# Kernel tuning notes

Hardware: AMD Instinct MI355X
Metric: run time of the kernel (lower is better)

Reference implementation:

```python
import jax, jax.numpy as jnp
import numpy as np

EPS = 1e-6  # floor

def setup_inputs() -> dict:
    key = jax.random.key(0)
    k1, = jax.random.split(key, 1)
    # mel-spectrogram magnitudes: non-negative
    x = jax.random.uniform(k1, (64, 2048, 160, 1), dtype=jnp.float32)  # [B,T,F,C]
    alpha = jnp.array([0.98], dtype=jnp.float32)
    smooth = jnp.array([0.03], dtype=jnp.float32)
    delta = jnp.array([2.0], dtype=jnp.float32)
    root = jnp.array([0.5], dtype=jnp.float32)
    return {"x": x, "alpha": alpha, "smooth": smooth, "delta": delta, "root": root}

def reference(x, alpha, smooth, delta, root):
    # EMA recurrence over time: m[t] = (1 - s) * x[t] + s * m[t-1], m[-1] = 0
    xt = jnp.swapaxes(x, 0, 1)  # [T,B,F,C]

    def step(prev, cur):
        new = (1.0 - smooth) * cur + smooth * prev
        return new, new

    _, smoothed_t = jax.lax.scan(step, jnp.zeros_like(xt[0]), xt)
    smoothed = jnp.swapaxes(smoothed_t, 0, 1)  # [B,T,F,C]

    # PCEN: (x / (eps + M)^alpha + delta)^root - delta^root
    pcen = (x / (EPS + smoothed) ** alpha + delta) ** root - delta ** root
    return pcen
```

## Files before the change

### kernel.cpp

```cpp
#include <hip/hip_runtime.h>
#include <stdint.h>

#define EPS 1e-6f

constexpr int Bq   = 64;
constexpr int Tq   = 2048;
constexpr int Fq   = 160;
constexpr int FQ4  = 40;
constexpr int ROWS = 64;
constexpr int WARM = 8;
constexpr int CH   = 8;
constexpr int TPB  = 320;
constexpr int NTILE = Tq / ROWS;
constexpr int NWG   = Bq * NTILE;
constexpr int TILE_ROWS  = ROWS + WARM;
constexpr int TILE_BYTES = TILE_ROWS * Fq * 4;
constexpr int MAIN_BYTES = ROWS * Fq * 4;

typedef float f4 __attribute__((ext_vector_type(4)));

__device__ __forceinline__ float fast_pow_pos(float b, float e) {
    return __builtin_amdgcn_exp2f(e * __builtin_amdgcn_logf(b));
}

template<bool RSQ>
__device__ __forceinline__ float pcen_one(float xv, float h, float na, float oms,
                                          float r, float d, float droot) {
    float me    = fmaf(oms, h, EPS);
    float ratio = xv * __builtin_amdgcn_exp2f(na * __builtin_amdgcn_logf(me));
    if (RSQ) return __builtin_amdgcn_sqrtf(ratio + d) - droot;
    else     return fast_pow_pos(ratio + d, r) - droot;
}

__device__ __forceinline__ void load_lds_16(const void* g, void* l) {
    __builtin_amdgcn_global_load_lds(
        (const unsigned int __attribute__((address_space(1)))*)(uintptr_t)g,
        (unsigned int __attribute__((address_space(3)))*)(uint32_t)(uintptr_t)l,
        16, 0, 0);
}

template<bool RSQ>
__device__ __forceinline__ void main_loop(const float* __restrict__ lds,
                                          int c, int f, f4 h,
                                          float s, float oms, float na,
                                          float r, float d, float droot,
                                          f4* __restrict__ outr, int gbase) {
#pragma unroll
    for (int j = 0; j < CH; ++j) {
        f4 xv = *(const f4*)&lds[(WARM + c * CH + j) * Fq + f * 4];
        h.x = fmaf(s, h.x, xv.x);
        h.y = fmaf(s, h.y, xv.y);
        h.z = fmaf(s, h.z, xv.z);
        h.w = fmaf(s, h.w, xv.w);
        f4 o;
        o.x = pcen_one<RSQ>(xv.x, h.x, na, oms, r, d, droot);
        o.y = pcen_one<RSQ>(xv.y, h.y, na, oms, r, d, droot);
        o.z = pcen_one<RSQ>(xv.z, h.z, na, oms, r, d, droot);
        o.w = pcen_one<RSQ>(xv.w, h.w, na, oms, r, d, droot);
        __builtin_nontemporal_store(o, &outr[gbase + j * FQ4]);
    }
}

__global__ __launch_bounds__(TPB) void pcen_kernel(
    const float* __restrict__ x,
    const float* __restrict__ alpha_p,
    const float* __restrict__ smooth_p,
    const float* __restrict__ delta_p,
    const float* __restrict__ root_p,
    float* __restrict__ out)
{
    __shared__ __align__(16) float lds[TILE_ROWS * Fq];

    const int wg    = ((blockIdx.x & 7) << 8) | (blockIdx.x >> 3);
    const int tile  = wg % NTILE;
    const int b     = wg / NTILE;
    const int r0    = b * Tq + tile * ROWS;
    const bool first = (tile == 0);

    const int wave = threadIdx.x >> 6;
    const int lane = threadIdx.x & 63;

    {
        const char* src = (const char*)(x + (size_t)(first ? r0 : r0 - WARM) * Fq);
        char*       dst = (char*)lds + (first ? WARM * Fq * 4 : 0);
        const int   per = (first ? MAIN_BYTES : TILE_BYTES) / 1024 / 5;
        for (int i = 0; i < per; ++i) {
            const int off = (wave + 5 * i) * 1024;
            load_lds_16(src + off + lane * 16, dst + off);
        }
    }

    const float s     = smooth_p[0];
    const float a     = alpha_p[0];
    const float d     = delta_p[0];
    const float r     = root_p[0];
    const float oms   = 1.0f - s;
    const float na    = -a;
    const bool  rsq   = (r == 0.5f);
    const float droot = rsq ? __builtin_amdgcn_sqrtf(d) : fast_pow_pos(d, r);

    __syncthreads();

    const int f = threadIdx.x % FQ4;
    const int c = threadIdx.x / FQ4;

    f4 h = (f4){0.f, 0.f, 0.f, 0.f};

    if (!(first && c == 0)) {
#pragma unroll
        for (int j = 0; j < WARM; ++j) {
            f4 xv = *(const f4*)&lds[(c * CH + j) * Fq + f * 4];
            h.x = fmaf(s, h.x, xv.x);
            h.y = fmaf(s, h.y, xv.y);
            h.z = fmaf(s, h.z, xv.z);
            h.w = fmaf(s, h.w, xv.w);
        }
    }

    f4* __restrict__ outr = (f4*)out;
    const int gbase = (r0 + c * CH) * FQ4 + f;

    if (rsq) main_loop<true >(lds, c, f, h, s, oms, na, r, d, droot, outr, gbase);
    else     main_loop<false>(lds, c, f, h, s, oms, na, r, d, droot, outr, gbase);
}

extern "C" void kernel_launch(void* const* d_in, const int* in_sizes, int n_in,
                              void* d_out, int out_size, void* d_ws, size_t ws_size,
                              hipStream_t stream) {
    const float* x      = (const float*)d_in[0];
    const float* alpha  = (const float*)d_in[1];
    const float* smooth = (const float*)d_in[2];
    const float* delta  = (const float*)d_in[3];
    const float* root   = (const float*)d_in[4];
    float* out          = (float*)d_out;

    pcen_kernel<<<NWG, TPB, 0, stream>>>(x, alpha, smooth, delta, root, out);
}
```

Measured before the change: 156.8 us.

## Process four time tiles per block with double-buffered LDS prefetch

```diff
diff --git a/kernel.cpp b/kernel.cpp
--- a/kernel.cpp
+++ b/kernel.cpp
@@ -12,12 +12,16 @@
 constexpr int CH   = 8;
 constexpr int TPB  = 320;
 constexpr int NTILE = Tq / ROWS;
-constexpr int NWG   = Bq * NTILE;
-constexpr int TILE_ROWS  = ROWS + WARM;
-constexpr int TILE_BYTES = TILE_ROWS * Fq * 4;
-constexpr int MAIN_BYTES = ROWS * Fq * 4;
+constexpr int TPG   = 4;
+constexpr int QUADS = NTILE / TPG;
+constexpr int BLKS  = Bq * QUADS;
+constexpr int TILE_F = ROWS * Fq;
 
 typedef float f4 __attribute__((ext_vector_type(4)));
+
+#define SCHED0() __builtin_amdgcn_sched_barrier(0)
+#define BAR() do { SCHED0(); __builtin_amdgcn_s_barrier(); SCHED0(); } while (0)
+#define WAIT_VM8() do { asm volatile("s_waitcnt vmcnt(8)" ::: "memory"); SCHED0(); } while (0)
 
 __device__ __forceinline__ float fast_pow_pos(float b, float e) {
     return __builtin_amdgcn_exp2f(e * __builtin_amdgcn_logf(b));
@@ -32,6 +36,13 @@
     else     return fast_pow_pos(ratio + d, r) - droot;
 }
 
+__device__ __forceinline__ void ema4(f4& h, const f4 xv, float s) {
+    h.x = fmaf(s, h.x, xv.x);
+    h.y = fmaf(s, h.y, xv.y);
+    h.z = fmaf(s, h.z, xv.z);
+    h.w = fmaf(s, h.w, xv.w);
+}
+
 __device__ __forceinline__ void load_lds_16(const void* g, void* l) {
     __builtin_amdgcn_global_load_lds(
         (const unsigned int __attribute__((address_space(1)))*)(uintptr_t)g,
@@ -40,24 +51,75 @@
 }
 
 template<bool RSQ>
-__device__ __forceinline__ void main_loop(const float* __restrict__ lds,
-                                          int c, int f, f4 h,
-                                          float s, float oms, float na,
-                                          float r, float d, float droot,
-                                          f4* __restrict__ outr, int gbase) {
+__device__ __forceinline__ void run(
+    const float* __restrict__ x, float* __restrict__ out,
+    float (* __restrict__ lds)[TILE_F],
+    int r00, bool gwarm, int f, int c, int wave, int lane,
+    float s, float oms, float na, float r, float d, float droot)
+{
+    f4* __restrict__ outr = (f4*)out;
+
+    auto stage = [&](int p, int row0) {
+        const char* src = (const char*)(x + (size_t)row0 * Fq);
+        char*       dst = (char*)&lds[p][0];
 #pragma unroll
-    for (int j = 0; j < CH; ++j) {
-        f4 xv = *(const f4*)&lds[(WARM + c * CH + j) * Fq + f * 4];
-        h.x = fmaf(s, h.x, xv.x);
-        h.y = fmaf(s, h.y, xv.y);
-        h.z = fmaf(s, h.z, xv.z);
-        h.w = fmaf(s, h.w, xv.w);
-        f4 o;
-        o.x = pcen_one<RSQ>(xv.x, h.x, na, oms, r, d, droot);
-        o.y = pcen_one<RSQ>(xv.y, h.y, na, oms, r, d, droot);
-        o.z = pcen_one<RSQ>(xv.z, h.z, na, oms, r, d, droot);
-        o.w = pcen_one<RSQ>(xv.w, h.w, na, oms, r, d, droot);
-        __builtin_nontemporal_store(o, &outr[gbase + j * FQ4]);
+        for (int i = 0; i < 8; ++i) {
+            const int off = (wave + 5 * i) * 1024;
+            load_lds_16(src + off + lane * 16, dst + off);
+        }
+    };
+
+    stage(0, r00);
+
+    f4 wreg[WARM];
+    if (c == 0 && gwarm) {
+        const float* wb = x + (size_t)(r00 - WARM) * Fq + f * 4;
+#pragma unroll
+        for (int j = 0; j < WARM; ++j) wreg[j] = *(const f4*)(wb + j * Fq);
+    }
+
+#pragma unroll
+    for (int t = 0; t < TPG; ++t) {
+        const int p  = t & 1;
+        const int r0 = r00 + t * ROWS;
+
+        f4 h = (f4){0.f, 0.f, 0.f, 0.f};
+        if (c == 0) {
+            if (t == 0) {
+                if (gwarm) {
+#pragma unroll
+                    for (int j = 0; j < WARM; ++j) ema4(h, wreg[j], s);
+                }
+            } else {
+#pragma unroll
+                for (int j = 0; j < WARM; ++j)
+                    ema4(h, *(const f4*)&lds[1 - p][(ROWS - WARM + j) * Fq + f * 4], s);
+            }
+        }
+
+        BAR();
+        if (t + 1 < TPG) stage(1 - p, r0 + ROWS);
+        WAIT_VM8();
+        BAR();
+
+        if (c > 0) {
+#pragma unroll
+            for (int j = 0; j < WARM; ++j)
+                ema4(h, *(const f4*)&lds[p][((c - 1) * CH + j) * Fq + f * 4], s);
+        }
+
+        const int gb = (r0 + c * CH) * FQ4 + f;
+#pragma unroll
+        for (int j = 0; j < CH; ++j) {
+            f4 xv = *(const f4*)&lds[p][(c * CH + j) * Fq + f * 4];
+            ema4(h, xv, s);
+            f4 o;
+            o.x = pcen_one<RSQ>(xv.x, h.x, na, oms, r, d, droot);
+            o.y = pcen_one<RSQ>(xv.y, h.y, na, oms, r, d, droot);
+            o.z = pcen_one<RSQ>(xv.z, h.z, na, oms, r, d, droot);
+            o.w = pcen_one<RSQ>(xv.w, h.w, na, oms, r, d, droot);
+            __builtin_nontemporal_store(o, &outr[gb + j * FQ4]);
+        }
     }
 }
 
@@ -69,26 +131,17 @@
     const float* __restrict__ root_p,
     float* __restrict__ out)
 {
-    __shared__ __align__(16) float lds[TILE_ROWS * Fq];
+    __shared__ __align__(16) float lds[2][TILE_F];
 
-    const int wg    = ((blockIdx.x & 7) << 8) | (blockIdx.x >> 3);
-    const int tile  = wg % NTILE;
-    const int b     = wg / NTILE;
-    const int r0    = b * Tq + tile * ROWS;
-    const bool first = (tile == 0);
+    const int bid = ((blockIdx.x & 7) << 6) | (blockIdx.x >> 3);
+    const int b   = bid / QUADS;
+    const int qd  = bid % QUADS;
+    const int r00 = b * Tq + qd * (TPG * ROWS);
 
+    const int f    = threadIdx.x % FQ4;
+    const int c    = threadIdx.x / FQ4;
     const int wave = threadIdx.x >> 6;
     const int lane = threadIdx.x & 63;
-
-    {
-        const char* src = (const char*)(x + (size_t)(first ? r0 : r0 - WARM) * Fq);
-        char*       dst = (char*)lds + (first ? WARM * Fq * 4 : 0);
-        const int   per = (first ? MAIN_BYTES : TILE_BYTES) / 1024 / 5;
-        for (int i = 0; i < per; ++i) {
-            const int off = (wave + 5 * i) * 1024;
-            load_lds_16(src + off + lane * 16, dst + off);
-        }
-    }
 
     const float s     = smooth_p[0];
     const float a     = alpha_p[0];
@@ -98,30 +151,12 @@
     const float na    = -a;
     const bool  rsq   = (r == 0.5f);
     const float droot = rsq ? __builtin_amdgcn_sqrtf(d) : fast_pow_pos(d, r);
+    const bool  gwarm = (qd > 0);
 
-    __syncthreads();
-
-    const int f = threadIdx.x % FQ4;
-    const int c = threadIdx.x / FQ4;
-
-    f4 h = (f4){0.f, 0.f, 0.f, 0.f};
-
-    if (!(first && c == 0)) {
-#pragma unroll
-        for (int j = 0; j < WARM; ++j) {
-            f4 xv = *(const f4*)&lds[(c * CH + j) * Fq + f * 4];
-            h.x = fmaf(s, h.x, xv.x);
-            h.y = fmaf(s, h.y, xv.y);
-            h.z = fmaf(s, h.z, xv.z);
-            h.w = fmaf(s, h.w, xv.w);
-        }
-    }
-
-    f4* __restrict__ outr = (f4*)out;
-    const int gbase = (r0 + c * CH) * FQ4 + f;
-
-    if (rsq) main_loop<true >(lds, c, f, h, s, oms, na, r, d, droot, outr, gbase);
-    else     main_loop<false>(lds, c, f, h, s, oms, na, r, d, droot, outr, gbase);
+    if (rsq) run<true >(x, out, lds, r00, gwarm, f, c, wave, lane,
+                        s, oms, na, r, d, droot);
+    else     run<false>(x, out, lds, r00, gwarm, f, c, wave, lane,
+                        s, oms, na, r, d, droot);
 }
 
 extern "C" void kernel_launch(void* const* d_in, const int* in_sizes, int n_in,
@@ -134,5 +169,5 @@
     const float* root   = (const float*)d_in[4];
     float* out          = (float*)d_out;
 
-    pcen_kernel<<<NWG, TPB, 0, stream>>>(x, alpha, smooth, delta, root, out);
+    pcen_kernel<<<BLKS, TPB, 0, stream>>>(x, alpha, smooth, delta, root, out);
 }
```

Measured after the change: 159.3 us. No clear change (+1.6%).
